# Performance work log

Measured on AMD Instinct MI355X. Metric: run time of the kernel, lower is better.

The kernel has to match this reference:

```python
import jax, jax.numpy as jnp
import numpy as np

V, H, B, T = 32000, 1024, 64, 512
EPS = 1e-5


def setup_inputs() -> dict:
    key = jax.random.key(0)
    ks = jax.random.split(key, 12)
    s = lambda i, shape: (jax.random.normal(ks[i], shape, dtype=jnp.float32) * 0.02)
    inp = {
        "x": jax.random.randint(ks[0], (B, T), 0, V),
        "t": jax.random.uniform(ks[1], (B,), dtype=jnp.float32),
        "emb": s(2, (V, H)),
        "w_ih1": s(3, (4 * H, H)), "w_hh1": s(4, (4 * H, H)),
        "b_ih1": jnp.zeros((4 * H,), jnp.float32), "b_hh1": jnp.zeros((4 * H,), jnp.float32),
        "gamma1": jnp.ones((H,), jnp.float32), "beta1": jnp.zeros((H,), jnp.float32),
        "w_ih2": s(5, (4 * H, H)), "w_hh2": s(6, (4 * H, H)),
        "b_ih2": jnp.zeros((4 * H,), jnp.float32), "b_hh2": jnp.zeros((4 * H,), jnp.float32),
        "gamma2": jnp.ones((H,), jnp.float32), "beta2": jnp.zeros((H,), jnp.float32),
        "fc_w": s(7, (1, H)), "fc_b": jnp.zeros((1,), jnp.float32),
        # LockedDropout: one mask per layer, reused at every timestep, pre-scaled by 1/keep
        "mask1": jax.random.bernoulli(ks[8], 0.5, (B, H)).astype(jnp.float32) / 0.5,
        "mask2": jax.random.bernoulli(ks[9], 0.7, (B, H)).astype(jnp.float32) / 0.7,
    }
    return inp


def _lstm_step(xt, h, c, w_ih, w_hh, b_ih, b_hh):
    # PyTorch LSTMCell gate order: i, f, g, o
    g = xt @ w_ih.T + h @ w_hh.T + (b_ih + b_hh)
    i, f, gg, o = jnp.split(g, 4, axis=-1)
    c = jax.nn.sigmoid(f) * c + jax.nn.sigmoid(i) * jnp.tanh(gg)
    h = jax.nn.sigmoid(o) * jnp.tanh(c)
    return h, c


def _bn(x, gamma, beta):
    # BatchNorm1d in training mode: per-feature batch stats (biased variance)
    m = x.mean(0)
    v = x.var(0)
    return gamma * (x - m) * jax.lax.rsqrt(v + EPS) + beta


def reference(x, t, emb, w_ih1, w_hh1, b_ih1, b_hh1, gamma1, beta1,
              w_ih2, w_hh2, b_ih2, b_hh2, gamma2, beta2, fc_w, fc_b,
              mask1, mask2):
    e = emb[x]                      # [B, T, H]
    e = jnp.transpose(e, (1, 0, 2)) # [T, B, H]

    def step(carry, et):
        h1, c1, h2, c2 = carry
        h1, c1 = _lstm_step(et, h1, c1, w_ih1, w_hh1, b_ih1, b_hh1)
        o = _bn(h1, gamma1, beta1) * mask1
        h2, c2 = _lstm_step(o, h2, c2, w_ih2, w_hh2, b_ih2, b_hh2)
        o = _bn(h2, gamma2, beta2) * mask2
        return (h1, c1, h2, c2), o

    z = jnp.zeros((B, H), jnp.float32)
    _, outs = jax.lax.scan(step, (z, z, z, z), e)  # outs: [T, B, H]

    pooled = outs.max(axis=0)                      # MaxPool1d over time -> [B, H]
    logits = (pooled @ fc_w.T + fc_b)[:, 0]        # [B]
    # BCEWithLogitsLoss (mean), numerically stable
    loss = jnp.mean(jnp.maximum(logits, 0.0) - logits * t + jnp.log1p(jnp.exp(-jnp.abs(logits))))
    return (loss, logits)
```

## Files before the change

kernel.cpp:

```cpp
#include <hip/hip_runtime.h>

#define HDIM  1024
#define BDIM  64
#define TDIM  512
#define FRAGB 131072
#define FRAGE 65536
#define SLOTS 4
#define NGRP  8

typedef __bf16 bf16x8 __attribute__((ext_vector_type(8)));
typedef float  f32x4  __attribute__((ext_vector_type(4)));
typedef int    i32x4  __attribute__((ext_vector_type(4)));

#define MFMA(a, b, c) __builtin_amdgcn_mfma_f32_16x16x32_bf16(a, b, c, 0, 0, 0)

#define GL(dst, p, off) \
    asm volatile("global_load_dwordx4 %0, %1, off offset:" off " sc0 sc1" \
                 : "=v"(dst) : "v"(p) : "memory")
#define GLF16(f, p) do { \
    const char* p0_ = (const char*)(p); \
    const char* p1_ = p0_ + 4096; const char* p2_ = p0_ + 8192; const char* p3_ = p0_ + 12288; \
    GL(f[0],  p0_, "0"); GL(f[1],  p0_, "1024"); GL(f[2],  p0_, "2048"); GL(f[3],  p0_, "3072"); \
    GL(f[4],  p1_, "0"); GL(f[5],  p1_, "1024"); GL(f[6],  p1_, "2048"); GL(f[7],  p1_, "3072"); \
    GL(f[8],  p2_, "0"); GL(f[9],  p2_, "1024"); GL(f[10], p2_, "2048"); GL(f[11], p2_, "3072"); \
    GL(f[12], p3_, "0"); GL(f[13], p3_, "1024"); GL(f[14], p3_, "2048"); GL(f[15], p3_, "3072"); \
} while (0)
#define WAITV() asm volatile("s_waitcnt vmcnt(0)" ::: "memory")
#define GS16(p, v) \
    asm volatile("global_store_dwordx4 %0, %1, off sc0 sc1" :: "v"(p), "v"(v) : "memory")

__device__ __forceinline__ float sigf(float x) {
    return __builtin_amdgcn_rcpf(1.0f + __builtin_amdgcn_exp2f(-1.44269504f * x));
}
__device__ __forceinline__ float tanh_fast(float x) {
    return 2.0f * __builtin_amdgcn_rcpf(1.0f + __builtin_amdgcn_exp2f(-2.88539008f * x)) - 1.0f;
}

__device__ __forceinline__ bf16x8 cvt8(const float* p) {
    const f32x4* q = (const f32x4*)p;
    f32x4 a = q[0], b = q[1];
    bf16x8 r;
    r[0] = (__bf16)a[0]; r[1] = (__bf16)a[1]; r[2] = (__bf16)a[2]; r[3] = (__bf16)a[3];
    r[4] = (__bf16)b[0]; r[5] = (__bf16)b[1]; r[6] = (__bf16)b[2]; r[7] = (__bf16)b[3];
    return r;
}

__device__ __forceinline__ void wspin(const int* base) {
    int l = threadIdx.x & 63;
    const int* p = (l < 8) ? base + l * 16 : nullptr;
    for (;;) {
        int v = p ? __hip_atomic_load(p, __ATOMIC_RELAXED, __HIP_MEMORY_SCOPE_AGENT) : 16;
        if (__all(v >= 16)) break;
        __builtin_amdgcn_s_sleep(1);
    }
}
__device__ __forceinline__ void spin1(const int* c, int n) {
    if (threadIdx.x == 0)
        while (__hip_atomic_load(c, __ATOMIC_RELAXED, __HIP_MEMORY_SCOPE_AGENT) < n)
            __builtin_amdgcn_s_sleep(1);
    __syncthreads();
}

__device__ __forceinline__ void gemm16r(const char* pa,
                                        const bf16x8 (&w0)[16], const bf16x8 (&w1)[16],
                                        f32x4& c00, f32x4& c01, f32x4& c10, f32x4& c11) {
#pragma unroll
    for (int i = 0; i < 16; i++) {
        bf16x8 a0v = *(const bf16x8*)(pa + i * 1024);
        bf16x8 a1v = *(const bf16x8*)(pa + 32768 + i * 1024);
        c00 = MFMA(a0v, w0[i], c00); c01 = MFMA(a0v, w1[i], c01);
        c10 = MFMA(a1v, w0[i], c10); c11 = MFMA(a1v, w1[i], c11);
    }
}

__global__ void gather_emb(const int* __restrict__ x, const float* __restrict__ emb,
                           __bf16* __restrict__ xseqfrag) {
    int t = blockIdx.x;
    for (int u = threadIdx.x; u < 8192; u += 256) {
        int lane = u & 63, c = (u >> 6) & 31, bt = u >> 11;
        int row = lane & 15, quad = lane >> 4;
        int b = bt * 16 + row, k = c * 32 + quad * 8;
        int tok = x[b * TDIM + t];
        bf16x8 r = cvt8(emb + (size_t)tok * HDIM + k);
        *(bf16x8*)(xseqfrag + (size_t)t * FRAGE + (size_t)u * 8) = r;
    }
}

template <int BIG>
__global__ void __launch_bounds__(512, 2) rnn_all(
    const int* __restrict__ x, const float* __restrict__ tv,
    const float* __restrict__ emb,
    const float* __restrict__ w_ih1, const float* __restrict__ w_hh1,
    const float* __restrict__ b_ih1, const float* __restrict__ b_hh1,
    const float* __restrict__ gamma1, const float* __restrict__ beta1,
    const float* __restrict__ w_ih2, const float* __restrict__ w_hh2,
    const float* __restrict__ b_ih2, const float* __restrict__ b_hh2,
    const float* __restrict__ gamma2, const float* __restrict__ beta2,
    const float* __restrict__ fc_w, const float* __restrict__ fc_b,
    const float* __restrict__ mask1, const float* __restrict__ mask2,
    const __bf16* __restrict__ xseq, int use_xseq,
    int* __restrict__ l1h, int* __restrict__ l1o, int* __restrict__ l2h,
    int* __restrict__ poolg, const char* __restrict__ hzero,
    char* __restrict__ h1p, char* __restrict__ h2p, char* __restrict__ o1p,
    float* __restrict__ pooled, float* __restrict__ out) {
    __shared__ float bias_s[32];
    __shared__ float gbufX0[32 * 68];
    __shared__ float gbufX1[32 * 68];
    __shared__ float gbufH0[32 * 68];
    __shared__ float gbufH1[32 * 68];
    __shared__ float xh[8 * 68];
    __shared__ float stat_m[8], stat_r[8];
    __shared__ __align__(16) __bf16 hstage[512];
    __shared__ __align__(16) __bf16 ostage[512];

    const int tid   = threadIdx.x;
    const int layer = blockIdx.x & 1;
    const int lb    = blockIdx.x >> 1;
    const int grp   = lb >> 4;
    const int fbase = lb * 8;

    const float* w_ih = layer ? w_ih2 : w_ih1;
    const float* w_hh = layer ? w_hh2 : w_hh1;
    const float* b_ih = layer ? b_ih2 : b_ih1;
    const float* b_hh = layer ? b_hh2 : b_hh1;
    const float* gam_ = layer ? gamma2 : gamma1;
    const float* bet_ = layer ? beta2  : beta1;
    const float* msk_ = layer ? mask2  : mask1;

    if (tid < 32) {
        int row = (tid >> 3) * HDIM + fbase + (tid & 7);
        bias_s[tid] = b_ih[row] + b_hh[row];
    }
    __syncthreads();
    if (BIG)
        __builtin_amdgcn_fence(__ATOMIC_ACQUIRE, "agent");

    const int lane = tid & 63;
    const int wv   = tid >> 6;
    const int bh   = wv & 1;
    const int kh   = (wv >> 1) & 1;
    const int g    = wv >> 2;
    const int qm   = lane & 15;
    const int quad = lane >> 4;
    const int aoff = (bh * 64 + kh * 16) * 1024 + lane * 16;

    bf16x8 wr0[16], wr1[16];
    {
        const float* wsrc = g ? w_hh : w_ih;
        const float* p0 = wsrc + (size_t)((qm >> 3) * HDIM + fbase + (qm & 7)) * HDIM
                               + kh * 512 + quad * 8;
        const float* p1 = wsrc + (size_t)(((16 + qm) >> 3) * HDIM + fbase + (qm & 7)) * HDIM
                               + kh * 512 + quad * 8;
#pragma unroll
        for (int i = 0; i < 16; i++) {
            wr0[i] = cvt8(p0 + i * 32);
            wr1[i] = cvt8(p1 + i * 32);
        }
    }

    const int bb = tid >> 3, jj = tid & 7;
    const int feat = fbase + jj;
    const float gv = gam_[feat], bev = bet_[feat], mv = msk_[bb * HDIM + feat];
    float cst = 0.0f, pmax = -1e30f;

    const int soff = (((lane >> 4) * 32 + (lb >> 2)) * 64 + ((lb & 3) * 16 + (lane & 15))) * 16;

    char* h_self = layer ? h2p : h1p;
    int*  ch     = layer ? l2h : l1h;

#pragma unroll 1
    for (int t = 0; t < TDIM; t++) {
        f32x4 a00 = {0.f,0.f,0.f,0.f}, a01 = {0.f,0.f,0.f,0.f};
        f32x4 a10 = {0.f,0.f,0.f,0.f}, a11 = {0.f,0.f,0.f,0.f};

        if (g == 0) {
            if (layer == 0) {
                if (use_xseq) {
                    gemm16r((const char*)xseq + (size_t)t * FRAGB + aoff, wr0, wr1,
                            a00, a01, a10, a11);
                } else {
                    const float* pe0 = emb + (size_t)x[(bh*32 + qm)*TDIM + t]*HDIM + kh*512 + quad*8;
                    const float* pe1 = emb + (size_t)x[(bh*32 + 16 + qm)*TDIM + t]*HDIM + kh*512 + quad*8;
#pragma unroll 4
                    for (int i = 0; i < 16; i++) {
                        bf16x8 v0 = cvt8(pe0 + i * 32), v1 = cvt8(pe1 + i * 32);
                        a00 = MFMA(v0, wr0[i], a00); a01 = MFMA(v0, wr1[i], a01);
                        a10 = MFMA(v1, wr0[i], a10); a11 = MFMA(v1, wr1[i], a11);
                    }
                }
            } else {
                wspin(l1o + (size_t)t * NGRP * 16);
                if (BIG) {
                    gemm16r(o1p + (size_t)t * FRAGB + aoff, wr0, wr1, a00, a01, a10, a11);
                } else {
                    const char* p = o1p + (size_t)(t & (SLOTS - 1)) * FRAGB + aoff;
                    bf16x8 f[16];
                    GLF16(f, p); WAITV();
#pragma unroll
                    for (int i = 0; i < 16; i++) {
                        a00 = MFMA(f[i], wr0[i], a00); a01 = MFMA(f[i], wr1[i], a01);
                    }
                    GLF16(f, p + 32768); WAITV();
#pragma unroll
                    for (int i = 0; i < 16; i++) {
                        a10 = MFMA(f[i], wr0[i], a10); a11 = MFMA(f[i], wr1[i], a11);
                    }
                }
            }
        } else {
            if (t >= 1) wspin(ch + (size_t)(t - 1) * NGRP * 16);
            if (BIG) {
                const char* src = (t == 0) ? hzero : (const char*)(h_self + (size_t)(t - 1) * FRAGB);
                gemm16r(src + aoff, wr0, wr1, a00, a01, a10, a11);
            } else {
                const char* p = h_self + (size_t)(t & 1) * FRAGB + aoff;
                bf16x8 f[16];
                GLF16(f, p); WAITV();
#pragma unroll
                for (int i = 0; i < 16; i++) {
                    a00 = MFMA(f[i], wr0[i], a00); a01 = MFMA(f[i], wr1[i], a01);
                }
                GLF16(f, p + 32768); WAITV();
#pragma unroll
                for (int i = 0; i < 16; i++) {
                    a10 = MFMA(f[i], wr0[i], a10); a11 = MFMA(f[i], wr1[i], a11);
                }
            }
        }

        float* myg = g ? (kh ? gbufH1 : gbufH0) : (kh ? gbufX1 : gbufX0);
        const int r0  = bh * 32 + quad * 4;
        const int i00 = qm * 68 + r0, i01 = (16 + qm) * 68 + r0;
        if (!g && !kh) {
            float b0 = bias_s[qm], b1 = bias_s[16 + qm];
            f32x4 s0 = {b0, b0, b0, b0}, s1 = {b1, b1, b1, b1};
            a00 += s0; a01 += s1; a10 += s0; a11 += s1;
        }
        *(f32x4*)&myg[i00]      = a00;
        *(f32x4*)&myg[i01]      = a01;
        *(f32x4*)&myg[i00 + 16] = a10;
        *(f32x4*)&myg[i01 + 16] = a11;
        __syncthreads();

        const int cb = jj * 68 + bb;
        float gi = gbufX0[cb] + gbufX1[cb] + gbufH0[cb] + gbufH1[cb];
        float gf = gbufX0[cb + 8*68] + gbufX1[cb + 8*68] + gbufH0[cb + 8*68] + gbufH1[cb + 8*68];
        float gg = gbufX0[cb + 16*68] + gbufX1[cb + 16*68] + gbufH0[cb + 16*68] + gbufH1[cb + 16*68];
        float go = gbufX0[cb + 24*68] + gbufX1[cb + 24*68] + gbufH0[cb + 24*68] + gbufH1[cb + 24*68];
        cst = sigf(gf) * cst + sigf(gi) * tanh_fast(gg);
        float h = sigf(go) * tanh_fast(cst);
        hstage[tid] = (__bf16)h;
        xh[jj * 68 + bb] = h;
        __syncthreads();

        size_t hslot = BIG ? (size_t)t * FRAGB : (size_t)((t + 1) & 1) * FRAGB;
        if (wv == 0) {
            i32x4 val = *(const i32x4*)(hstage + lane * 8);
            GS16(h_self + hslot + soff, val);
        }
        float v = xh[wv * 68 + lane];
        float s1 = v, s2 = v * v;
#pragma unroll
        for (int off = 32; off; off >>= 1) {
            s1 += __shfl_xor(s1, off);
            s2 += __shfl_xor(s2, off);
        }
        if (lane == 0) {
            float m  = s1 * (1.0f / 64.0f);
            float va = s2 * (1.0f / 64.0f) - m * m;
            stat_m[wv] = m;
            stat_r[wv] = rsqrtf(va + 1e-5f);
        }
        if (wv == 0) {
            WAITV();
            if (lane == 0)
                __hip_atomic_fetch_add(ch + ((size_t)t * NGRP + grp) * 16, 1,
                                       __ATOMIC_RELAXED, __HIP_MEMORY_SCOPE_AGENT);
        }
        __syncthreads();

        float o = ((h - stat_m[jj]) * stat_r[jj] * gv + bev) * mv;
        if (layer == 0) {
            ostage[tid] = (__bf16)o;
            __syncthreads();
            if (wv == 1) {
                if (!BIG && t >= SLOTS)
                    wspin(l2h + (size_t)(t - SLOTS) * NGRP * 16);
                i32x4 val = *(const i32x4*)(ostage + lane * 8);
                size_t oslot = BIG ? (size_t)t * FRAGB : (size_t)(t & (SLOTS - 1)) * FRAGB;
                GS16(o1p + oslot + soff, val);
                WAITV();
                if (lane == 0)
                    __hip_atomic_fetch_add(l1o + ((size_t)t * NGRP + grp) * 16, 1,
                                           __ATOMIC_RELAXED, __HIP_MEMORY_SCOPE_AGENT);
            }
        } else {
            pmax = fmaxf(pmax, o);
        }
    }

    if (layer == 1) {
        __hip_atomic_store(&pooled[bb * HDIM + feat], pmax,
                           __ATOMIC_RELAXED, __HIP_MEMORY_SCOPE_AGENT);
        WAITV();
        __syncthreads();
        if (tid == 0)
            __hip_atomic_fetch_add(poolg, 1, __ATOMIC_RELAXED, __HIP_MEMORY_SCOPE_AGENT);

        if (lb == 0) {
            spin1(poolg, 128);
            __builtin_amdgcn_fence(__ATOMIC_ACQUIRE, "agent");
            int b  = wv * 8 + (lane >> 3);
            int l8 = lane & 7;
            float s = 0.0f;
            for (int f = l8 * 128; f < l8 * 128 + 128; f++)
                s += pooled[b * HDIM + f] * fc_w[f];
            s += __shfl_xor(s, 1); s += __shfl_xor(s, 2); s += __shfl_xor(s, 4);
            float logit = s + fc_b[0];
            if (l8 == 0) {
                out[1 + b] = logit;
                gbufX0[b] = fmaxf(logit, 0.0f) - logit * tv[b] + log1pf(expf(-fabsf(logit)));
            }
            __syncthreads();
            if (tid < 64) {
                float term = gbufX0[tid];
#pragma unroll
                for (int off = 32; off; off >>= 1) term += __shfl_xor(term, off);
                if (tid == 0) out[0] = term * (1.0f / 64.0f);
            }
        }
    }
}

extern "C" void kernel_launch(void* const* d_in, const int* in_sizes, int n_in,
                              void* d_out, int out_size, void* d_ws, size_t ws_size,
                              hipStream_t stream) {
    const int*   x    = (const int*)d_in[0];
    const float* tv   = (const float*)d_in[1];
    const float* emb  = (const float*)d_in[2];
    const float* wih1 = (const float*)d_in[3];
    const float* whh1 = (const float*)d_in[4];
    const float* bih1 = (const float*)d_in[5];
    const float* bhh1 = (const float*)d_in[6];
    const float* g1   = (const float*)d_in[7];
    const float* be1  = (const float*)d_in[8];
    const float* wih2 = (const float*)d_in[9];
    const float* whh2 = (const float*)d_in[10];
    const float* bih2 = (const float*)d_in[11];
    const float* bhh2 = (const float*)d_in[12];
    const float* g2   = (const float*)d_in[13];
    const float* be2  = (const float*)d_in[14];
    const float* fcw  = (const float*)d_in[15];
    const float* fcb  = (const float*)d_in[16];
    const float* m1   = (const float*)d_in[17];
    const float* m2   = (const float*)d_in[18];

    char* w = (char*)d_ws;
    float* out = (float*)d_out;

    const size_t SEQB = (size_t)TDIM * FRAGB;
    size_t boff = 0;
    int*   B_l1h   = (int*)(w + boff); boff += 262144;
    int*   B_l1o   = (int*)(w + boff); boff += 262144;
    int*   B_l2h   = (int*)(w + boff); boff += 262144;
    int*   B_poolg = (int*)(w + boff); boff += 4096;
    char*  B_hzero = w + boff;         boff += FRAGB;
    size_t B_msz   = boff;
    char*  B_h1    = w + boff;         boff += SEQB;
    char*  B_h2    = w + boff;         boff += SEQB;
    char*  B_o1    = w + boff;         boff += SEQB;
    float* B_pool  = (float*)(w + boff); boff += 262144;
    __bf16* B_xseq = (__bf16*)(w + boff); boff += SEQB;
    size_t need_big = boff;

    if (ws_size >= need_big) {
        hipMemsetAsync(d_ws, 0, B_msz, stream);
        gather_emb<<<dim3(TDIM), dim3(256), 0, stream>>>(x, emb, B_xseq);
        int use_xseq = 1;
        void* args[] = {&x, &tv, &emb, &wih1, &whh1, &bih1, &bhh1, &g1, &be1,
                        &wih2, &whh2, &bih2, &bhh2, &g2, &be2, &fcw, &fcb, &m1, &m2,
                        (void*)&B_xseq, &use_xseq,
                        &B_l1h, &B_l1o, &B_l2h, &B_poolg, (void*)&B_hzero,
                        &B_h1, &B_h2, &B_o1, &B_pool, &out};
        hipLaunchCooperativeKernel((void*)rnn_all<1>, dim3(256), dim3(512), args, 0, stream);
        return;
    }

    int*    l1h    = (int*)(w);
    int*    l1o    = (int*)(w + 262144);
    int*    l2h    = (int*)(w + 524288);
    int*    poolg  = (int*)(w + 786432);
    char*   hzero  = w;
    char*   h1frag = w + 790528;
    char*   h2frag = h1frag + 262144;
    char*   o1frag = h2frag + 262144;
    float*  pooled = (float*)(o1frag + 524288);
    __bf16* xseq   = (__bf16*)((char*)pooled + 262144);
    size_t fixed   = (size_t)((char*)xseq - w);
    int use_xseq = (ws_size >= fixed + SEQB) ? 1 : 0;

    hipMemsetAsync(d_ws, 0, fixed, stream);
    if (use_xseq)
        gather_emb<<<dim3(TDIM), dim3(256), 0, stream>>>(x, emb, xseq);

    void* args[] = {&x, &tv, &emb, &wih1, &whh1, &bih1, &bhh1, &g1, &be1,
                    &wih2, &whh2, &bih2, &bhh2, &g2, &be2, &fcw, &fcb, &m1, &m2,
                    (void*)&xseq, &use_xseq,
                    &l1h, &l1o, &l2h, &poolg, (void*)&hzero,
                    &h1frag, &h2frag, &o1frag, &pooled, &out};
    hipLaunchCooperativeKernel((void*)rnn_all<0>, dim3(256), dim3(512), args, 0, stream);
}
```

Before: 3.767 ms.

## Replace per-group counters with per-block flags and consume K-chunks as they arrive

```diff
diff --git a/kernel.cpp b/kernel.cpp
--- a/kernel.cpp
+++ b/kernel.cpp
@@ -7,6 +7,8 @@
 #define FRAGE 65536
 #define SLOTS 4
 #define NGRP  8
+#define FLI(t, g) (((size_t)(t) * NGRP + (g)) * 32)
+#define FLBYTES   (TDIM * NGRP * 32 * 4)
 
 typedef __bf16 bf16x8 __attribute__((ext_vector_type(8)));
 typedef float  f32x4  __attribute__((ext_vector_type(4)));
@@ -17,14 +19,6 @@
 #define GL(dst, p, off) \
     asm volatile("global_load_dwordx4 %0, %1, off offset:" off " sc0 sc1" \
                  : "=v"(dst) : "v"(p) : "memory")
-#define GLF16(f, p) do { \
-    const char* p0_ = (const char*)(p); \
-    const char* p1_ = p0_ + 4096; const char* p2_ = p0_ + 8192; const char* p3_ = p0_ + 12288; \
-    GL(f[0],  p0_, "0"); GL(f[1],  p0_, "1024"); GL(f[2],  p0_, "2048"); GL(f[3],  p0_, "3072"); \
-    GL(f[4],  p1_, "0"); GL(f[5],  p1_, "1024"); GL(f[6],  p1_, "2048"); GL(f[7],  p1_, "3072"); \
-    GL(f[8],  p2_, "0"); GL(f[9],  p2_, "1024"); GL(f[10], p2_, "2048"); GL(f[11], p2_, "3072"); \
-    GL(f[12], p3_, "0"); GL(f[13], p3_, "1024"); GL(f[14], p3_, "2048"); GL(f[15], p3_, "3072"); \
-} while (0)
 #define WAITV() asm volatile("s_waitcnt vmcnt(0)" ::: "memory")
 #define GS16(p, v) \
     asm volatile("global_store_dwordx4 %0, %1, off sc0 sc1" :: "v"(p), "v"(v) : "memory")
@@ -45,14 +39,26 @@
     return r;
 }
 
-__device__ __forceinline__ void wspin(const int* base) {
+__device__ __forceinline__ void wspin_g(const int* f) {
+    const int* p = f + (threadIdx.x & 15);
+    for (;;) {
+        int v = __hip_atomic_load(p, __ATOMIC_RELAXED, __HIP_MEMORY_SCOPE_AGENT);
+        if (__all(v != 0)) break;
+        __builtin_amdgcn_s_sleep(1);
+    }
+    asm volatile("" ::: "memory");
+}
+__device__ __forceinline__ void wspin8(const int* base) {
     int l = threadIdx.x & 63;
-    const int* p = (l < 8) ? base + l * 16 : nullptr;
+    const int* p1 = base + (l >> 4) * 32 + (l & 15);
+    const int* p2 = base + 128 + (l >> 4) * 32 + (l & 15);
     for (;;) {
-        int v = p ? __hip_atomic_load(p, __ATOMIC_RELAXED, __HIP_MEMORY_SCOPE_AGENT) : 16;
-        if (__all(v >= 16)) break;
+        int v1 = __hip_atomic_load(p1, __ATOMIC_RELAXED, __HIP_MEMORY_SCOPE_AGENT);
+        int v2 = __hip_atomic_load(p2, __ATOMIC_RELAXED, __HIP_MEMORY_SCOPE_AGENT);
+        if (__all((v1 != 0) && (v2 != 0))) break;
         __builtin_amdgcn_s_sleep(1);
     }
+    asm volatile("" ::: "memory");
 }
 __device__ __forceinline__ void spin1(const int* c, int n) {
     if (threadIdx.x == 0)
@@ -60,6 +66,9 @@
             __builtin_amdgcn_s_sleep(1);
     __syncthreads();
 }
+__device__ __forceinline__ void post_flag(int* f) {
+    __hip_atomic_store(f, 1, __ATOMIC_RELAXED, __HIP_MEMORY_SCOPE_AGENT);
+}
 
 __device__ __forceinline__ void gemm16r(const char* pa,
                                         const bf16x8 (&w0)[16], const bf16x8 (&w1)[16],
@@ -70,6 +79,35 @@
         bf16x8 a1v = *(const bf16x8*)(pa + 32768 + i * 1024);
         c00 = MFMA(a0v, w0[i], c00); c01 = MFMA(a0v, w1[i], c01);
         c10 = MFMA(a1v, w0[i], c10); c11 = MFMA(a1v, w1[i], c11);
+    }
+}
+__device__ __forceinline__ void gemm_grp(const char* pa, int gg,
+                                         const bf16x8 (&w0)[16], const bf16x8 (&w1)[16],
+                                         f32x4& c00, f32x4& c01, f32x4& c10, f32x4& c11) {
+#pragma unroll
+    for (int k = 0; k < 4; k++) {
+        int i = gg * 4 + k;
+        bf16x8 a0v = *(const bf16x8*)(pa + i * 1024);
+        bf16x8 a1v = *(const bf16x8*)(pa + 32768 + i * 1024);
+        c00 = MFMA(a0v, w0[i], c00); c01 = MFMA(a0v, w1[i], c01);
+        c10 = MFMA(a1v, w0[i], c10); c11 = MFMA(a1v, w1[i], c11);
+    }
+}
+__device__ __forceinline__ void gemm_grp_gl(const char* pa, int gg,
+                                            const bf16x8 (&w0)[16], const bf16x8 (&w1)[16],
+                                            f32x4& c00, f32x4& c01, f32x4& c10, f32x4& c11) {
+    bf16x8 f0[4], f1[4];
+#pragma unroll
+    for (int k = 0; k < 4; k++) {
+        GL(f0[k], pa + (gg * 4 + k) * 1024, "0");
+        GL(f1[k], pa + 32768 + (gg * 4 + k) * 1024, "0");
+    }
+    WAITV();
+#pragma unroll
+    for (int k = 0; k < 4; k++) {
+        int i = gg * 4 + k;
+        c00 = MFMA(f0[k], w0[i], c00); c01 = MFMA(f0[k], w1[i], c01);
+        c10 = MFMA(f1[k], w0[i], c10); c11 = MFMA(f1[k], w1[i], c11);
     }
 }
 
@@ -117,6 +155,7 @@
     const int layer = blockIdx.x & 1;
     const int lb    = blockIdx.x >> 1;
     const int grp   = lb >> 4;
+    const int slot16 = lb & 15;
     const int fbase = lb * 8;
 
     const float* w_ih = layer ? w_ih2 : w_ih1;
@@ -189,42 +228,21 @@
                     }
                 }
             } else {
-                wspin(l1o + (size_t)t * NGRP * 16);
-                if (BIG) {
-                    gemm16r(o1p + (size_t)t * FRAGB + aoff, wr0, wr1, a00, a01, a10, a11);
-                } else {
-                    const char* p = o1p + (size_t)(t & (SLOTS - 1)) * FRAGB + aoff;
-                    bf16x8 f[16];
-                    GLF16(f, p); WAITV();
-#pragma unroll
-                    for (int i = 0; i < 16; i++) {
-                        a00 = MFMA(f[i], wr0[i], a00); a01 = MFMA(f[i], wr1[i], a01);
-                    }
-                    GLF16(f, p + 32768); WAITV();
-#pragma unroll
-                    for (int i = 0; i < 16; i++) {
-                        a10 = MFMA(f[i], wr0[i], a10); a11 = MFMA(f[i], wr1[i], a11);
-                    }
+                const char* p = BIG ? o1p + (size_t)t * FRAGB + aoff
+                                    : o1p + (size_t)(t & (SLOTS - 1)) * FRAGB + aoff;
+                for (int gg = 0; gg < 4; gg++) {
+                    wspin_g(l1o + FLI(t, kh * 4 + gg));
+                    if (BIG) gemm_grp   (p, gg, wr0, wr1, a00, a01, a10, a11);
+                    else     gemm_grp_gl(p, gg, wr0, wr1, a00, a01, a10, a11);
                 }
             }
-        } else {
-            if (t >= 1) wspin(ch + (size_t)(t - 1) * NGRP * 16);
-            if (BIG) {
-                const char* src = (t == 0) ? hzero : (const char*)(h_self + (size_t)(t - 1) * FRAGB);
-                gemm16r(src + aoff, wr0, wr1, a00, a01, a10, a11);
-            } else {
-                const char* p = h_self + (size_t)(t & 1) * FRAGB + aoff;
-                bf16x8 f[16];
-                GLF16(f, p); WAITV();
-#pragma unroll
-                for (int i = 0; i < 16; i++) {
-                    a00 = MFMA(f[i], wr0[i], a00); a01 = MFMA(f[i], wr1[i], a01);
-                }
-                GLF16(f, p + 32768); WAITV();
-#pragma unroll
-                for (int i = 0; i < 16; i++) {
-                    a10 = MFMA(f[i], wr0[i], a10); a11 = MFMA(f[i], wr1[i], a11);
-                }
+        } else if (t >= 1) {
+            const char* p = BIG ? (const char*)(h_self + (size_t)(t - 1) * FRAGB) + aoff
+                                : (const char*)(h_self + (size_t)(t & 1) * FRAGB) + aoff;
+            for (int gg = 0; gg < 4; gg++) {
+                wspin_g(ch + FLI(t - 1, kh * 4 + gg));
+                if (BIG) gemm_grp   (p, gg, wr0, wr1, a00, a01, a10, a11);
+                else     gemm_grp_gl(p, gg, wr0, wr1, a00, a01, a10, a11);
             }
         }
 
@@ -274,8 +292,7 @@
         if (wv == 0) {
             WAITV();
             if (lane == 0)
-                __hip_atomic_fetch_add(ch + ((size_t)t * NGRP + grp) * 16, 1,
-                                       __ATOMIC_RELAXED, __HIP_MEMORY_SCOPE_AGENT);
+                post_flag(ch + FLI(t, grp) + slot16);
         }
         __syncthreads();
 
@@ -285,14 +302,13 @@
             __syncthreads();
             if (wv == 1) {
                 if (!BIG && t >= SLOTS)
-                    wspin(l2h + (size_t)(t - SLOTS) * NGRP * 16);
+                    wspin8(l2h + FLI(t - SLOTS, 0));
                 i32x4 val = *(const i32x4*)(ostage + lane * 8);
                 size_t oslot = BIG ? (size_t)t * FRAGB : (size_t)(t & (SLOTS - 1)) * FRAGB;
                 GS16(o1p + oslot + soff, val);
                 WAITV();
                 if (lane == 0)
-                    __hip_atomic_fetch_add(l1o + ((size_t)t * NGRP + grp) * 16, 1,
-                                           __ATOMIC_RELAXED, __HIP_MEMORY_SCOPE_AGENT);
+                    post_flag(l1o + FLI(t, grp) + slot16);
             }
         } else {
             pmax = fmaxf(pmax, o);
@@ -360,9 +376,9 @@
 
     const size_t SEQB = (size_t)TDIM * FRAGB;
     size_t boff = 0;
-    int*   B_l1h   = (int*)(w + boff); boff += 262144;
-    int*   B_l1o   = (int*)(w + boff); boff += 262144;
-    int*   B_l2h   = (int*)(w + boff); boff += 262144;
+    int*   B_l1h   = (int*)(w + boff); boff += FLBYTES;
+    int*   B_l1o   = (int*)(w + boff); boff += FLBYTES;
+    int*   B_l2h   = (int*)(w + boff); boff += FLBYTES;
     int*   B_poolg = (int*)(w + boff); boff += 4096;
     char*  B_hzero = w + boff;         boff += FRAGB;
     size_t B_msz   = boff;
@@ -386,15 +402,17 @@
         return;
     }
 
-    int*    l1h    = (int*)(w);
-    int*    l1o    = (int*)(w + 262144);
-    int*    l2h    = (int*)(w + 524288);
-    int*    poolg  = (int*)(w + 786432);
+    size_t soff2 = 0;
+    int*    l1h    = (int*)(w + soff2); soff2 += FLBYTES;
+    int*    l1o    = (int*)(w + soff2); soff2 += FLBYTES;
+    int*    l2h    = (int*)(w + soff2); soff2 += FLBYTES;
+    int*    poolg  = (int*)(w + soff2); soff2 += 4096;
     char*   hzero  = w;
-    char*   h1frag = w + 790528;
-    char*   h2frag = h1frag + 262144;
-    char*   o1frag = h2frag + 262144;
-    float*  pooled = (float*)(o1frag + 524288);
+    char*   h1frag = w + soff2;         soff2 += 2 * FRAGB;
+    char*   h2frag = w + (soff2 - 0);   soff2 += 0;
+    h2frag = h1frag + 2 * FRAGB;        soff2 = (size_t)(h2frag - w) + 2 * FRAGB;
+    char*   o1frag = h2frag + 2 * FRAGB; soff2 = (size_t)(o1frag - w) + SLOTS * FRAGB;
+    float*  pooled = (float*)(o1frag + SLOTS * FRAGB);
     __bf16* xseq   = (__bf16*)((char*)pooled + 262144);
     size_t fixed   = (size_t)((char*)xseq - w);
     int use_xseq = (ws_size >= fixed + SEQB) ? 1 : 0;
```

Result: no change. 3.827 ms (+1.6%).
